# Performance work log

Measured on AMD Instinct MI355X. Metric: run time of the kernel, lower is better.

The kernel has to match this reference:

```python
import jax, jax.numpy as jnp
import numpy as np

N = 50000
E = 800000
IN_DIM = 128
HID = 32
OUT_DIM = 64
HEADS = 4
NEG_SLOPE = 0.2  # DGL GATConv default leaky_relu slope


def setup_inputs() -> dict:
    key = jax.random.key(0)
    ks = jax.random.split(key, 16)
    h = jax.random.normal(ks[0], (N, IN_DIM), dtype=jnp.float32)
    src = jax.random.randint(ks[1], (E,), 0, N, dtype=jnp.int32)
    dst = jax.random.randint(ks[2], (E,), 0, N, dtype=jnp.int32)
    s = 0.05
    # layer 1: in 128 -> heads*32 = 128
    W1 = jax.random.normal(ks[3], (IN_DIM, HEADS * HID), dtype=jnp.float32) * s
    al1 = jax.random.normal(ks[4], (HEADS, HID), dtype=jnp.float32) * s
    ar1 = jax.random.normal(ks[5], (HEADS, HID), dtype=jnp.float32) * s
    # layer 2: in 128 -> heads*32 = 128
    W2 = jax.random.normal(ks[6], (HEADS * HID, HEADS * HID), dtype=jnp.float32) * s
    al2 = jax.random.normal(ks[7], (HEADS, HID), dtype=jnp.float32) * s
    ar2 = jax.random.normal(ks[8], (HEADS, HID), dtype=jnp.float32) * s
    # last layer: in 128 -> heads*64 = 256 (needs residual projection)
    W3 = jax.random.normal(ks[9], (HEADS * HID, HEADS * OUT_DIM), dtype=jnp.float32) * s
    al3 = jax.random.normal(ks[10], (HEADS, OUT_DIM), dtype=jnp.float32) * s
    ar3 = jax.random.normal(ks[11], (HEADS, OUT_DIM), dtype=jnp.float32) * s
    resW3 = jax.random.normal(ks[12], (HEADS * HID, HEADS * OUT_DIM), dtype=jnp.float32) * s
    return {"h": h, "W1": W1, "al1": al1, "ar1": ar1, "W2": W2, "al2": al2,
            "ar2": ar2, "W3": W3, "al3": al3, "ar3": ar3, "resW3": resW3,
            "src": src, "dst": dst}


def gat_layer(h, src, dst, W, al, ar, heads, out_feats, res_W=None, act=None):
    n = h.shape[0]
    feat = (h @ W).reshape(n, heads, out_feats)          # [N,H,D]
    el = jnp.einsum('nhd,hd->nh', feat, al)               # [N,H]
    er = jnp.einsum('nhd,hd->nh', feat, ar)               # [N,H]
    e = jax.nn.leaky_relu(el[src] + er[dst], NEG_SLOPE)   # [E,H]
    m = jax.ops.segment_max(e, dst, num_segments=n)       # per-dst max, [N,H]
    ex = jnp.exp(e - m[dst])
    denom = jax.ops.segment_sum(ex, dst, num_segments=n)  # [N,H]
    alpha = ex / denom[dst]                               # edge softmax, [E,H]
    msg = feat[src] * alpha[:, :, None]                   # [E,H,D]
    rst = jax.ops.segment_sum(msg, dst, num_segments=n)   # [N,H,D]
    res = (h @ res_W) if res_W is not None else h
    rst = rst + res.reshape(n, heads, out_feats)
    if act is not None:
        rst = act(rst)
    return rst


def reference(h, W1, al1, ar1, W2, al2, ar2, W3, al3, ar3, resW3, src, dst):
    n = h.shape[0]
    x = gat_layer(h, src, dst, W1, al1, ar1, HEADS, HID, act=jax.nn.relu)
    x = x.reshape(n, -1)
    # feat_drop=0.3 on layer 2 omitted (eval/deterministic mode)
    x = gat_layer(x, src, dst, W2, al2, ar2, HEADS, HID, act=jax.nn.relu)
    x = x.reshape(n, -1)
    x = gat_layer(x, src, dst, W3, al3, ar3, HEADS, OUT_DIM, res_W=resW3)
    return x.mean(axis=1)  # mean over heads -> [N, OUT_DIM]
```

## Files before the change

### kernel.cpp

```cpp
#include <hip/hip_runtime.h>
#include <hip/hip_bf16.h>
#include <math.h>


#define NEG_SLOPE 0.2f

typedef __attribute__((ext_vector_type(8))) __bf16 bf16x8;
typedef __attribute__((ext_vector_type(4))) float f32x4;

__device__ __forceinline__ float leaky(float x) { return fmaxf(x, NEG_SLOPE * x); }
__device__ __forceinline__ ushort f2bf(float f) {
    unsigned u = __float_as_uint(f);
    return (ushort)((u + 0x7fffu + ((u >> 16) & 1u)) >> 16);
}
__device__ __forceinline__ float bf2f(ushort b) { return __uint_as_float(((unsigned)b) << 16); }
__device__ __forceinline__ float lo16f(unsigned v) { return __uint_as_float(v << 16); }
__device__ __forceinline__ float hi16f(unsigned v) { return __uint_as_float(v & 0xffff0000u); }


__global__ void hist_kernel(const int* __restrict__ dst, int* __restrict__ deg, int E) {
    int i = blockIdx.x * blockDim.x + threadIdx.x;
    if (i < E) atomicAdd(&deg[dst[i]], 1);
}

__global__ void block_scan_kernel(const int* __restrict__ deg, int* __restrict__ loc,
                                  int* __restrict__ bsum, int n) {
    __shared__ int sm[1024];
    const int tid = threadIdx.x;
    const int i = blockIdx.x * 1024 + tid;
    int v = (i < n) ? deg[i] : 0;
    sm[tid] = v;
    __syncthreads();
    for (int off = 1; off < 1024; off <<= 1) {
        int t = (tid >= off) ? sm[tid - off] : 0;
        __syncthreads();
        sm[tid] += t;
        __syncthreads();
    }
    if (i < n) loc[i] = sm[tid] - v;
    if (tid == 1023) bsum[blockIdx.x] = sm[1023];
}

__global__ void scan_bsum_kernel(int* __restrict__ bsum, int nb, int* __restrict__ total_out) {
    const int lane = threadIdx.x;
    int v = (lane < nb) ? bsum[lane] : 0;
    int orig = v;
    for (int off = 1; off < 64; off <<= 1) {
        int t = __shfl_up(v, off);
        if (lane >= off) v += t;
    }
    if (lane < nb) bsum[lane] = v - orig;
    if (lane == 63) *total_out = v;
}

__global__ void apply_scan_kernel(const int* __restrict__ loc, const int* __restrict__ bsum,
                                  int* __restrict__ row_ptr, int* __restrict__ cursor, int n) {
    int i = blockIdx.x * blockDim.x + threadIdx.x;
    if (i < n) {
        int v = loc[i] + bsum[i >> 10];
        row_ptr[i] = v;
        cursor[i]  = v;
    }
}

__global__ void scatter_kernel(const int* __restrict__ src, const int* __restrict__ dst,
                               int* __restrict__ cursor, int* __restrict__ ssrc, int E) {
    int i = blockIdx.x * blockDim.x + threadIdx.x;
    if (i < E) {
        int s = src[i];
        int pos = atomicAdd(&cursor[dst[i]], 1);
        ssrc[pos] = s;
    }
}


__global__ void prep_kernel(const float* __restrict__ h, ushort* __restrict__ xbh,
                            const float* __restrict__ W1, ushort* __restrict__ W1th,
                            const float* __restrict__ W2, ushort* __restrict__ W2th,
                            const float* __restrict__ W3, ushort* __restrict__ W3th,
                            const float* __restrict__ rW3, ushort* __restrict__ rWmh,
                            int nh4) {
    int i = blockIdx.x * blockDim.x + threadIdx.x;
    if (i < nh4) {
        float4 v = ((const float4*)h)[i];
        ushort4 o;
        o.x = f2bf(v.x); o.y = f2bf(v.y); o.z = f2bf(v.z); o.w = f2bf(v.w);
        ((ushort4*)xbh)[i] = o;
        return;
    }
    int j = i - nh4;
    if (j < 16384) {
        int c = j >> 7, k = j & 127;
        int kd = k ^ ((c & 7) << 3);
        W1th[c * 128 + kd] = f2bf(W1[k * 128 + c]);
    } else if (j < 32768) {
        j -= 16384;
        int c = j >> 7, k = j & 127;
        int kd = k ^ ((c & 7) << 3);
        W2th[c * 128 + kd] = f2bf(W2[k * 128 + c]);
    } else if (j < 65536) {
        j -= 32768;
        int c = j >> 7, k = j & 127;
        int kd = k ^ ((c & 7) << 3);
        W3th[c * 128 + kd] = f2bf(W3[k * 256 + c]);
    } else if (j < 73728) {
        j -= 65536;
        int c = j >> 7, k = j & 127;
        const float* row = rW3 + (size_t)k * 256;
        float v = 0.25f * ((row[c] + row[64 + c]) + (row[128 + c] + row[192 + c]));
        int kd = k ^ ((c & 7) << 3);
        rWmh[c * 128 + kd] = f2bf(v);
    }
}


__global__ void __launch_bounds__(256)
gemm_kernel(const ushort* __restrict__ Ah, const ushort* __restrict__ Bth,
            const ushort* __restrict__ B2th,
            ushort* __restrict__ Cb, float* __restrict__ C2f,
            const float* __restrict__ alv, const float* __restrict__ arv,
            float* __restrict__ el, float* __restrict__ er,
            int M, int Ncols, int dshift) {
    extern __shared__ ushort Ws[];
    ushort* Ws2 = Ws + 64 * 128;
    const int tid = threadIdx.x;
    const int wv = tid >> 6;
    const int lane = tid & 63;
    const int l15 = lane & 15;
    const int g = lane >> 4;
    const int bm = blockIdx.x * 128 + wv * 32;
    const int bn = blockIdx.y * 64;
    const bool do2 = (B2th != nullptr) && (blockIdx.y == 0);

    {
        const uint4* gh = (const uint4*)(Bth + (size_t)bn * 128);
        uint4* sh = (uint4*)Ws;
#pragma unroll
        for (int it = 0; it < 4; ++it) sh[it * 256 + tid] = gh[it * 256 + tid];
        if (do2) {
            const uint4* g2 = (const uint4*)B2th;
            uint4* s2 = (uint4*)Ws2;
#pragma unroll
            for (int it = 0; it < 4; ++it) s2[it * 256 + tid] = g2[it * 256 + tid];
        }
    }
    __syncthreads();

    const int m0 = bm + l15;
    const int m1 = bm + 16 + l15;
    const int mc0 = (m0 < M) ? m0 : (M - 1);
    const int mc1 = (m1 < M) ? m1 : (M - 1);
    bf16x8 xh[2][4];
#pragma unroll
    for (int kk = 0; kk < 4; ++kk) {
        xh[0][kk] = *(const bf16x8*)(Ah + (size_t)mc0 * 128 + kk * 32 + g * 8);
        xh[1][kk] = *(const bf16x8*)(Ah + (size_t)mc1 * 128 + kk * 32 + g * 8);
    }

    f32x4 acc[2][4] = {};
    f32x4 acc2[2][4] = {};
    const int swz = (l15 & 7) << 4;
#pragma unroll
    for (int n = 0; n < 4; ++n) {
        const int colb = (n * 16 + l15) * 256;
#pragma unroll
        for (int kk = 0; kk < 4; ++kk) {
            const int boff = colb + ((kk * 64 + g * 16) ^ swz);
            bf16x8 wh = *(const bf16x8*)((const char*)Ws + boff);
            acc[0][n] = __builtin_amdgcn_mfma_f32_16x16x32_bf16(wh, xh[0][kk], acc[0][n], 0, 0, 0);
            acc[1][n] = __builtin_amdgcn_mfma_f32_16x16x32_bf16(wh, xh[1][kk], acc[1][n], 0, 0, 0);
            if (do2) {
                bf16x8 w2 = *(const bf16x8*)((const char*)Ws2 + boff);
                acc2[0][n] = __builtin_amdgcn_mfma_f32_16x16x32_bf16(w2, xh[0][kk], acc2[0][n], 0, 0, 0);
                acc2[1][n] = __builtin_amdgcn_mfma_f32_16x16x32_bf16(w2, xh[1][kk], acc2[1][n], 0, 0, 0);
            }
        }
    }

#pragma unroll
    for (int mf = 0; mf < 2; ++mf) {
        const int m = (mf == 0) ? m0 : m1;
        const bool valid = (m < M);
        if (valid) {
            size_t ro = (size_t)m * Ncols;
#pragma unroll
            for (int n = 0; n < 4; ++n) {
                int col = bn + n * 16 + g * 4;
                ushort4 o;
                o.x = f2bf(acc[mf][n][0]); o.y = f2bf(acc[mf][n][1]);
                o.z = f2bf(acc[mf][n][2]); o.w = f2bf(acc[mf][n][3]);
                *(ushort4*)&Cb[ro + col] = o;
                if (do2) {
                    *(float4*)&C2f[(size_t)m * 64 + n * 16 + g * 4] =
                        make_float4(acc2[mf][n][0], acc2[mf][n][1],
                                    acc2[mf][n][2], acc2[mf][n][3]);
                }
            }
        }
        if (alv) {
            float e0 = 0.f, e1 = 0.f, r0 = 0.f, r1 = 0.f;
#pragma unroll
            for (int n = 0; n < 4; ++n) {
#pragma unroll
                for (int r = 0; r < 4; ++r) {
                    int col = n * 16 + g * 4 + r;
                    float c = acc[mf][n][r];
                    float av = alv[bn + col];
                    float bv = arv[bn + col];
                    if ((col >> dshift) == 0) { e0 += c * av; r0 += c * bv; }
                    else                      { e1 += c * av; r1 += c * bv; }
                }
            }
            e0 += __shfl_xor(e0, 16); e0 += __shfl_xor(e0, 32);
            e1 += __shfl_xor(e1, 16); e1 += __shfl_xor(e1, 32);
            r0 += __shfl_xor(r0, 16); r0 += __shfl_xor(r0, 32);
            r1 += __shfl_xor(r1, 16); r1 += __shfl_xor(r1, 32);
            if (valid && g == 0) {
                int h0 = bn >> dshift;
                el[m * 4 + h0] = e0;
                er[m * 4 + h0] = r0;
                if (dshift == 5) {
                    el[m * 4 + h0 + 1] = e1;
                    er[m * 4 + h0 + 1] = r1;
                }
            }
        }
    }
}


__global__ void __launch_bounds__(256)
aggregate12_kernel(const ushort* __restrict__ featb, const float* __restrict__ el,
                   const float* __restrict__ er, const int* __restrict__ row_ptr,
                   const int* __restrict__ ssrc, const float* __restrict__ resf,
                   const ushort* __restrict__ rxh, const ushort* __restrict__ rxl,
                   ushort* __restrict__ xbh, ushort* __restrict__ xbl, int n) {
    const int wid = threadIdx.x >> 6;
    const int lane = threadIdx.x & 63;
    const int node = blockIdx.x * 4 + wid;
    if (node >= n) return;
    const int beg = row_ptr[node];
    const int end = row_ptr[node + 1];
    const int hh = lane >> 4;
    const float erh = er[node * 4 + hh];

    float ssum = 0.f, a0 = 0.f, a1 = 0.f;
    int p = beg;
    for (; p + 8 <= end; p += 8) {
        int s[8];
        float e[8];
        unsigned v[8];
#pragma unroll
        for (int j = 0; j < 8; ++j) s[j] = __builtin_amdgcn_readfirstlane(ssrc[p + j]);
#pragma unroll
        for (int j = 0; j < 8; ++j) v[j] = *(const unsigned*)&featb[(size_t)s[j] * 128 + lane * 2];
#pragma unroll
        for (int j = 0; j < 8; ++j) e[j] = el[s[j] * 4 + hh];
#pragma unroll
        for (int j = 0; j < 8; ++j) {
            float w0 = __expf(leaky(e[j] + erh));
            ssum += w0;
            a0 += w0 * lo16f(v[j]);
            a1 += w0 * hi16f(v[j]);
        }
    }
    for (; p < end; ++p) {
        int s = __builtin_amdgcn_readfirstlane(ssrc[p]);
        float w0 = __expf(leaky(el[s * 4 + hh] + erh));
        unsigned v = *(const unsigned*)&featb[(size_t)s * 128 + lane * 2];
        ssum += w0;
        a0 += w0 * lo16f(v);
        a1 += w0 * hi16f(v);
    }
    float inv = (end > beg) ? 1.f / ssum : 0.f;
    size_t o = (size_t)node * 128 + lane * 2;
    float rb0, rb1;
    if (resf) {
        float2 f = *(const float2*)&resf[o];
        rb0 = f.x; rb1 = f.y;
    } else {
        unsigned rh = *(const unsigned*)&rxh[o];
        unsigned rl = *(const unsigned*)&rxl[o];
        rb0 = lo16f(rh) + lo16f(rl);
        rb1 = hi16f(rh) + hi16f(rl);
    }
    float r0 = fmaxf(a0 * inv + rb0, 0.f);
    float r1 = fmaxf(a1 * inv + rb1, 0.f);
    ushort h0 = f2bf(r0), h1 = f2bf(r1);
    ushort l0 = f2bf(r0 - bf2f(h0)), l1 = f2bf(r1 - bf2f(h1));
    *(unsigned*)&xbh[o] = (unsigned)h0 | ((unsigned)h1 << 16);
    *(unsigned*)&xbl[o] = (unsigned)l0 | ((unsigned)l1 << 16);
}


__global__ void __launch_bounds__(256)
aggregate3_kernel(const ushort* __restrict__ featb, const float* __restrict__ el,
                  const float* __restrict__ er, const int* __restrict__ row_ptr,
                  const int* __restrict__ ssrc, const float* __restrict__ resmean,
                  float* __restrict__ out, int n) {
    const int wid = threadIdx.x >> 6;
    const int lane = threadIdx.x & 63;
    const int node = blockIdx.x * 4 + wid;
    if (node >= n) return;
    const int beg = row_ptr[node];
    const int end = row_ptr[node + 1];
    const int hh = lane >> 4;
    const int dd = (lane & 15) * 4;
    const int off = hh * 64 + dd;
    const float erh = er[node * 4 + hh];

    float c0 = 0.f, c1 = 0.f, c2 = 0.f, c3 = 0.f, ssum = 0.f;
    int p = beg;
    for (; p + 8 <= end; p += 8) {
        int s[8];
        float e[8];
        uint2 v[8];
#pragma unroll
        for (int j = 0; j < 8; ++j) s[j] = __builtin_amdgcn_readfirstlane(ssrc[p + j]);
#pragma unroll
        for (int j = 0; j < 8; ++j) v[j] = *(const uint2*)&featb[(size_t)s[j] * 256 + off];
#pragma unroll
        for (int j = 0; j < 8; ++j) e[j] = el[s[j] * 4 + hh];
#pragma unroll
        for (int j = 0; j < 8; ++j) {
            float w0 = __expf(leaky(e[j] + erh));
            ssum += w0;
            c0 += w0 * lo16f(v[j].x);
            c1 += w0 * hi16f(v[j].x);
            c2 += w0 * lo16f(v[j].y);
            c3 += w0 * hi16f(v[j].y);
        }
    }
    for (; p < end; ++p) {
        int s = __builtin_amdgcn_readfirstlane(ssrc[p]);
        float w0 = __expf(leaky(el[s * 4 + hh] + erh));
        uint2 v = *(const uint2*)&featb[(size_t)s * 256 + off];
        ssum += w0;
        c0 += w0 * lo16f(v.x);
        c1 += w0 * hi16f(v.x);
        c2 += w0 * lo16f(v.y);
        c3 += w0 * hi16f(v.y);
    }
    float inv = (end > beg) ? 1.f / ssum : 0.f;
    float r0 = c0 * inv, r1 = c1 * inv, r2 = c2 * inv, r3 = c3 * inv;
    r0 += __shfl_xor(r0, 16); r0 += __shfl_xor(r0, 32);
    r1 += __shfl_xor(r1, 16); r1 += __shfl_xor(r1, 32);
    r2 += __shfl_xor(r2, 16); r2 += __shfl_xor(r2, 32);
    r3 += __shfl_xor(r3, 16); r3 += __shfl_xor(r3, 32);
    if (hh == 0) {
        float4 rm = *(const float4*)&resmean[(size_t)node * 64 + dd];
        *(float4*)&out[(size_t)node * 64 + dd] =
            make_float4(0.25f * r0 + rm.x, 0.25f * r1 + rm.y,
                        0.25f * r2 + rm.z, 0.25f * r3 + rm.w);
    }
}


extern "C" void kernel_launch(void* const* d_in, const int* in_sizes, int n_in,
                              void* d_out, int out_size, void* d_ws, size_t ws_size,
                              hipStream_t stream) {
    const float* h   = (const float*)d_in[0];
    const float* W1  = (const float*)d_in[1];
    const float* al1 = (const float*)d_in[2];
    const float* ar1 = (const float*)d_in[3];
    const float* W2  = (const float*)d_in[4];
    const float* al2 = (const float*)d_in[5];
    const float* ar2 = (const float*)d_in[6];
    const float* W3  = (const float*)d_in[7];
    const float* al3 = (const float*)d_in[8];
    const float* ar3 = (const float*)d_in[9];
    const float* rW3 = (const float*)d_in[10];
    const int* src   = (const int*)d_in[11];
    const int* dstv  = (const int*)d_in[12];
    const int N = in_sizes[0] / 128;
    const int E = in_sizes[11];
    float* out = (float*)d_out;

    char* p = (char*)d_ws;
    auto alloc = [&](size_t bytes) -> char* {
        char* q = p;
        p += (bytes + 255) & ~(size_t)255;
        return q;
    };
    int*    row_ptr = (int*)alloc((size_t)(N + 1) * 4);
    int*    cursor  = (int*)alloc((size_t)N * 4);
    int*    loc     = (int*)alloc((size_t)N * 4);
    int*    bsum    = (int*)alloc(64 * 4);
    int*    ssrc    = (int*)alloc((size_t)E * 4);
    float*  el      = (float*)alloc((size_t)N * 16);
    float*  er      = (float*)alloc((size_t)N * 16);
    ushort* featb   = (ushort*)alloc((size_t)N * 256 * 2);
    ushort* xbh     = (ushort*)alloc((size_t)N * 128 * 2);
    ushort* xbl     = (ushort*)alloc((size_t)N * 128 * 2);
    ushort* W1th = (ushort*)alloc(128 * 128 * 2);
    ushort* W2th = (ushort*)alloc(128 * 128 * 2);
    ushort* W3th = (ushort*)alloc(256 * 128 * 2);
    ushort* rWmh = (ushort*)alloc(64 * 128 * 2);
    float*  resmean = (float*)alloc((size_t)N * 64 * 4);

    hipMemsetAsync(cursor, 0, (size_t)N * 4, stream);
    hist_kernel<<<(E + 255) / 256, 256, 0, stream>>>(dstv, cursor, E);
    int nb = (N + 1023) / 1024;
    block_scan_kernel<<<nb, 1024, 0, stream>>>(cursor, loc, bsum, N);
    scan_bsum_kernel<<<1, 64, 0, stream>>>(bsum, nb, row_ptr + N);
    apply_scan_kernel<<<(N + 255) / 256, 256, 0, stream>>>(loc, bsum, row_ptr, cursor, N);
    scatter_kernel<<<(E + 255) / 256, 256, 0, stream>>>(src, dstv, cursor, ssrc, E);

    const int nh4 = N * 32;
    prep_kernel<<<(nh4 + 73728 + 255) / 256, 256, 0, stream>>>(
        h, xbh, W1, W1th, W2, W2th, W3, W3th, rW3, rWmh, nh4);

    const int gx = (N + 127) / 128;
    dim3 g1(gx, 2);
    dim3 g3(gx, 4);
    int agg_grid = (N + 3) / 4;
    const size_t lds1 = 64 * 128 * sizeof(ushort);
    const size_t lds2 = 2 * 64 * 128 * sizeof(ushort);

    gemm_kernel<<<g1, 256, lds1, stream>>>(xbh, W1th, nullptr, featb, nullptr,
                                           al1, ar1, el, er, N, 128, 5);
    aggregate12_kernel<<<agg_grid, 256, 0, stream>>>(featb, el, er, row_ptr, ssrc,
                                                     h, nullptr, nullptr, xbh, xbl, N);

    gemm_kernel<<<g1, 256, lds1, stream>>>(xbh, W2th, nullptr, featb, nullptr,
                                           al2, ar2, el, er, N, 128, 5);
    aggregate12_kernel<<<agg_grid, 256, 0, stream>>>(featb, el, er, row_ptr, ssrc,
                                                     nullptr, xbh, xbl, xbh, xbl, N);

    gemm_kernel<<<g3, 256, lds2, stream>>>(xbh, W3th, rWmh, featb, resmean,
                                           al3, ar3, el, er, N, 256, 6);
    aggregate3_kernel<<<agg_grid, 256, 0, stream>>>(featb, el, er, row_ptr, ssrc, resmean, out, N);
}
```

Before: 401.7 us.

## Widen GEMM column tile to 128, fold scan and memset into other kernels

The GEMM tile becomes 64 rows by 128 columns with 128 threads. Each block now covers all heads (layers 1-2) or two heads (layer 3), so activation rows are loaded once per column tile instead of per 64-column tile, and the el/er reductions cover four heads at once. The separate block-sum scan kernel is merged into apply_scan, and the cursor memset moves into the prep kernel, removing two launches. The cost is more LDS per block (32 KB, or 48 KB for layer 3), more accumulator registers, and fewer waves per block, which may lower occupancy.

After: 395.3 us. About the same (-1.6%).

```diff
diff --git a/kernel.cpp b/kernel.cpp
--- a/kernel.cpp
+++ b/kernel.cpp
@@ -41,23 +41,25 @@
     if (tid == 1023) bsum[blockIdx.x] = sm[1023];
 }
 
-__global__ void scan_bsum_kernel(int* __restrict__ bsum, int nb, int* __restrict__ total_out) {
-    const int lane = threadIdx.x;
-    int v = (lane < nb) ? bsum[lane] : 0;
-    int orig = v;
-    for (int off = 1; off < 64; off <<= 1) {
-        int t = __shfl_up(v, off);
-        if (lane >= off) v += t;
-    }
-    if (lane < nb) bsum[lane] = v - orig;
-    if (lane == 63) *total_out = v;
-}
-
 __global__ void apply_scan_kernel(const int* __restrict__ loc, const int* __restrict__ bsum,
-                                  int* __restrict__ row_ptr, int* __restrict__ cursor, int n) {
-    int i = blockIdx.x * blockDim.x + threadIdx.x;
+                                  int* __restrict__ row_ptr, int* __restrict__ cursor,
+                                  int n, int nb) {
+    __shared__ int pb[64];
+    const int tid = threadIdx.x;
+    if (tid < 64) {
+        int v = (tid < nb) ? bsum[tid] : 0;
+        int orig = v;
+        for (int off = 1; off < 64; off <<= 1) {
+            int t = __shfl_up(v, off);
+            if (tid >= off) v += t;
+        }
+        pb[tid] = v - orig;
+        if (tid == 63 && blockIdx.x == 0) row_ptr[n] = v;
+    }
+    __syncthreads();
+    int i = blockIdx.x * blockDim.x + tid;
     if (i < n) {
-        int v = loc[i] + bsum[i >> 10];
+        int v = loc[i] + pb[i >> 10];
         row_ptr[i] = v;
         cursor[i]  = v;
     }
@@ -79,7 +81,7 @@
                             const float* __restrict__ W2, ushort* __restrict__ W2th,
                             const float* __restrict__ W3, ushort* __restrict__ W3th,
                             const float* __restrict__ rW3, ushort* __restrict__ rWmh,
-                            int nh4) {
+                            int* __restrict__ cursor, int nh4, int n) {
     int i = blockIdx.x * blockDim.x + threadIdx.x;
     if (i < nh4) {
         float4 v = ((const float4*)h)[i];
@@ -110,11 +112,13 @@
         float v = 0.25f * ((row[c] + row[64 + c]) + (row[128 + c] + row[192 + c]));
         int kd = k ^ ((c & 7) << 3);
         rWmh[c * 128 + kd] = f2bf(v);
-    }
-}
-
-
-__global__ void __launch_bounds__(256)
+    } else if (j < 73728 + n) {
+        cursor[j - 73728] = 0;
+    }
+}
+
+
+__global__ void __launch_bounds__(128)
 gemm_kernel(const ushort* __restrict__ Ah, const ushort* __restrict__ Bth,
             const ushort* __restrict__ B2th,
             ushort* __restrict__ Cb, float* __restrict__ C2f,
@@ -122,26 +126,26 @@
             float* __restrict__ el, float* __restrict__ er,
             int M, int Ncols, int dshift) {
     extern __shared__ ushort Ws[];
-    ushort* Ws2 = Ws + 64 * 128;
+    ushort* Ws2 = Ws + 128 * 128;
     const int tid = threadIdx.x;
     const int wv = tid >> 6;
     const int lane = tid & 63;
     const int l15 = lane & 15;
     const int g = lane >> 4;
-    const int bm = blockIdx.x * 128 + wv * 32;
-    const int bn = blockIdx.y * 64;
+    const int bm = blockIdx.x * 64 + wv * 32;
+    const int bn = blockIdx.y * 128;
     const bool do2 = (B2th != nullptr) && (blockIdx.y == 0);
 
     {
         const uint4* gh = (const uint4*)(Bth + (size_t)bn * 128);
         uint4* sh = (uint4*)Ws;
 #pragma unroll
-        for (int it = 0; it < 4; ++it) sh[it * 256 + tid] = gh[it * 256 + tid];
+        for (int it = 0; it < 16; ++it) sh[it * 128 + tid] = gh[it * 128 + tid];
         if (do2) {
             const uint4* g2 = (const uint4*)B2th;
             uint4* s2 = (uint4*)Ws2;
 #pragma unroll
-            for (int it = 0; it < 4; ++it) s2[it * 256 + tid] = g2[it * 256 + tid];
+            for (int it = 0; it < 8; ++it) s2[it * 128 + tid] = g2[it * 128 + tid];
         }
     }
     __syncthreads();
@@ -157,11 +161,11 @@
         xh[1][kk] = *(const bf16x8*)(Ah + (size_t)mc1 * 128 + kk * 32 + g * 8);
     }
 
-    f32x4 acc[2][4] = {};
+    f32x4 acc[2][8] = {};
     f32x4 acc2[2][4] = {};
     const int swz = (l15 & 7) << 4;
 #pragma unroll
-    for (int n = 0; n < 4; ++n) {
+    for (int n = 0; n < 8; ++n) {
         const int colb = (n * 16 + l15) * 256;
 #pragma unroll
         for (int kk = 0; kk < 4; ++kk) {
@@ -169,7 +173,15 @@
             bf16x8 wh = *(const bf16x8*)((const char*)Ws + boff);
             acc[0][n] = __builtin_amdgcn_mfma_f32_16x16x32_bf16(wh, xh[0][kk], acc[0][n], 0, 0, 0);
             acc[1][n] = __builtin_amdgcn_mfma_f32_16x16x32_bf16(wh, xh[1][kk], acc[1][n], 0, 0, 0);
-            if (do2) {
+        }
+    }
+    if (do2) {
+#pragma unroll
+        for (int n = 0; n < 4; ++n) {
+            const int colb = (n * 16 + l15) * 256;
+#pragma unroll
+            for (int kk = 0; kk < 4; ++kk) {
+                const int boff = colb + ((kk * 64 + g * 16) ^ swz);
                 bf16x8 w2 = *(const bf16x8*)((const char*)Ws2 + boff);
                 acc2[0][n] = __builtin_amdgcn_mfma_f32_16x16x32_bf16(w2, xh[0][kk], acc2[0][n], 0, 0, 0);
                 acc2[1][n] = __builtin_amdgcn_mfma_f32_16x16x32_bf16(w2, xh[1][kk], acc2[1][n], 0, 0, 0);
@@ -184,13 +196,16 @@
         if (valid) {
             size_t ro = (size_t)m * Ncols;
 #pragma unroll
-            for (int n = 0; n < 4; ++n) {
+            for (int n = 0; n < 8; ++n) {
                 int col = bn + n * 16 + g * 4;
                 ushort4 o;
                 o.x = f2bf(acc[mf][n][0]); o.y = f2bf(acc[mf][n][1]);
                 o.z = f2bf(acc[mf][n][2]); o.w = f2bf(acc[mf][n][3]);
                 *(ushort4*)&Cb[ro + col] = o;
-                if (do2) {
+            }
+            if (do2) {
+#pragma unroll
+                for (int n = 0; n < 4; ++n) {
                     *(float4*)&C2f[(size_t)m * 64 + n * 16 + g * 4] =
                         make_float4(acc2[mf][n][0], acc2[mf][n][1],
                                     acc2[mf][n][2], acc2[mf][n][3]);
@@ -198,30 +213,49 @@
             }
         }
         if (alv) {
-            float e0 = 0.f, e1 = 0.f, r0 = 0.f, r1 = 0.f;
-#pragma unroll
-            for (int n = 0; n < 4; ++n) {
-#pragma unroll
-                for (int r = 0; r < 4; ++r) {
-                    int col = n * 16 + g * 4 + r;
-                    float c = acc[mf][n][r];
-                    float av = alv[bn + col];
-                    float bv = arv[bn + col];
-                    if ((col >> dshift) == 0) { e0 += c * av; r0 += c * bv; }
-                    else                      { e1 += c * av; r1 += c * bv; }
+            float e0 = 0.f, e1 = 0.f, e2 = 0.f, e3 = 0.f;
+            float r0 = 0.f, r1 = 0.f, r2 = 0.f, r3 = 0.f;
+            const bool four = (dshift == 5);
+#pragma unroll
+            for (int n = 0; n < 8; ++n) {
+                float se = 0.f, sr = 0.f;
+#pragma unroll
+                for (int rr = 0; rr < 4; ++rr) {
+                    int col = bn + n * 16 + g * 4 + rr;
+                    float c = acc[mf][n][rr];
+                    se += c * alv[col];
+                    sr += c * arv[col];
+                }
+                if (four) {
+                    if (n < 2)      { e0 += se; r0 += sr; }
+                    else if (n < 4) { e1 += se; r1 += sr; }
+                    else if (n < 6) { e2 += se; r2 += sr; }
+                    else            { e3 += se; r3 += sr; }
+                } else {
+                    if (n < 4)      { e0 += se; r0 += sr; }
+                    else            { e1 += se; r1 += sr; }
                 }
             }
             e0 += __shfl_xor(e0, 16); e0 += __shfl_xor(e0, 32);
             e1 += __shfl_xor(e1, 16); e1 += __shfl_xor(e1, 32);
             r0 += __shfl_xor(r0, 16); r0 += __shfl_xor(r0, 32);
             r1 += __shfl_xor(r1, 16); r1 += __shfl_xor(r1, 32);
+            if (four) {
+                e2 += __shfl_xor(e2, 16); e2 += __shfl_xor(e2, 32);
+                e3 += __shfl_xor(e3, 16); e3 += __shfl_xor(e3, 32);
+                r2 += __shfl_xor(r2, 16); r2 += __shfl_xor(r2, 32);
+                r3 += __shfl_xor(r3, 16); r3 += __shfl_xor(r3, 32);
+            }
             if (valid && g == 0) {
-                int h0 = bn >> dshift;
-                el[m * 4 + h0] = e0;
-                er[m * 4 + h0] = r0;
-                if (dshift == 5) {
-                    el[m * 4 + h0 + 1] = e1;
-                    er[m * 4 + h0 + 1] = r1;
+                if (four) {
+                    el[m * 4 + 0] = e0; el[m * 4 + 1] = e1;
+                    el[m * 4 + 2] = e2; el[m * 4 + 3] = e3;
+                    er[m * 4 + 0] = r0; er[m * 4 + 1] = r1;
+                    er[m * 4 + 2] = r2; er[m * 4 + 3] = r3;
+                } else {
+                    int h0 = bn >> 6;
+                    el[m * 4 + h0] = e0; el[m * 4 + h0 + 1] = e1;
+                    er[m * 4 + h0] = r0; er[m * 4 + h0 + 1] = r1;
                 }
             }
         }
@@ -398,36 +432,35 @@
     ushort* rWmh = (ushort*)alloc(64 * 128 * 2);
     float*  resmean = (float*)alloc((size_t)N * 64 * 4);
 
-    hipMemsetAsync(cursor, 0, (size_t)N * 4, stream);
+    const int nh4 = N * 32;
+    const int prep_total = nh4 + 73728 + N;
+    prep_kernel<<<(prep_total + 255) / 256, 256, 0, stream>>>(
+        h, xbh, W1, W1th, W2, W2th, W3, W3th, rW3, rWmh, cursor, nh4, N);
+
     hist_kernel<<<(E + 255) / 256, 256, 0, stream>>>(dstv, cursor, E);
     int nb = (N + 1023) / 1024;
     block_scan_kernel<<<nb, 1024, 0, stream>>>(cursor, loc, bsum, N);
-    scan_bsum_kernel<<<1, 64, 0, stream>>>(bsum, nb, row_ptr + N);
-    apply_scan_kernel<<<(N + 255) / 256, 256, 0, stream>>>(loc, bsum, row_ptr, cursor, N);
+    apply_scan_kernel<<<(N + 255) / 256, 256, 0, stream>>>(loc, bsum, row_ptr, cursor, N, nb);
     scatter_kernel<<<(E + 255) / 256, 256, 0, stream>>>(src, dstv, cursor, ssrc, E);
 
-    const int nh4 = N * 32;
-    prep_kernel<<<(nh4 + 73728 + 255) / 256, 256, 0, stream>>>(
-        h, xbh, W1, W1th, W2, W2th, W3, W3th, rW3, rWmh, nh4);
-
-    const int gx = (N + 127) / 128;
-    dim3 g1(gx, 2);
-    dim3 g3(gx, 4);
+    const int gx = (N + 63) / 64;
+    dim3 g1(gx, 1);
+    dim3 g3(gx, 2);
     int agg_grid = (N + 3) / 4;
-    const size_t lds1 = 64 * 128 * sizeof(ushort);
-    const size_t lds2 = 2 * 64 * 128 * sizeof(ushort);
-
-    gemm_kernel<<<g1, 256, lds1, stream>>>(xbh, W1th, nullptr, featb, nullptr,
+    const size_t lds1 = 128 * 128 * sizeof(ushort);
+    const size_t lds3 = (128 * 128 + 64 * 128) * sizeof(ushort);
+
+    gemm_kernel<<<g1, 128, lds1, stream>>>(xbh, W1th, nullptr, featb, nullptr,
                                            al1, ar1, el, er, N, 128, 5);
     aggregate12_kernel<<<agg_grid, 256, 0, stream>>>(featb, el, er, row_ptr, ssrc,
                                                      h, nullptr, nullptr, xbh, xbl, N);
 
-    gemm_kernel<<<g1, 256, lds1, stream>>>(xbh, W2th, nullptr, featb, nullptr,
+    gemm_kernel<<<g1, 128, lds1, stream>>>(xbh, W2th, nullptr, featb, nullptr,
                                            al2, ar2, el, er, N, 128, 5);
     aggregate12_kernel<<<agg_grid, 256, 0, stream>>>(featb, el, er, row_ptr, ssrc,
                                                      nullptr, xbh, xbl, xbh, xbl, N);
 
-    gemm_kernel<<<g3, 256, lds2, stream>>>(xbh, W3th, rWmh, featb, resmean,
+    gemm_kernel<<<g3, 128, lds3, stream>>>(xbh, W3th, rWmh, featb, resmean,
                                            al3, ar3, el, er, N, 256, 6);
     aggregate3_kernel<<<agg_grid, 256, 0, stream>>>(featb, el, er, row_ptr, ssrc, resmean, out, N);
 }
```
